# Kernel tuning notes

Measured on AMD Instinct MI355X. Metric: run time of the kernel, lower is better.

The kernel has to match this reference:

```python
import jax, jax.numpy as jnp
import numpy as np
from jax import lax


def _gru_layer(x, w_ih, w_hh, b_ih, b_hh):
    """PyTorch-style GRU layer (gate order r, z, n). x: [B,T,I] -> ([B,T,H], [B,H])."""
    B, T, _ = x.shape
    H = w_hh.shape[1]
    # Precompute all input-side gate projections in one big GEMM: [B,T,3H]
    xg = jnp.einsum('bti,gi->btg', x, w_ih) + b_ih

    def step(h, xg_t):
        hg = h @ w_hh.T + b_hh                      # [B,3H]
        xr, xz, xn = jnp.split(xg_t, 3, axis=-1)
        hr, hz, hn = jnp.split(hg, 3, axis=-1)
        r = jax.nn.sigmoid(xr + hr)
        z = jax.nn.sigmoid(xz + hz)
        n = jnp.tanh(xn + r * hn)
        h_new = (1.0 - z) * n + z * h
        return h_new, h_new

    h0 = jnp.zeros((B, H), dtype=x.dtype)
    h_last, hs = lax.scan(step, h0, jnp.swapaxes(xg, 0, 1))  # scan over time
    return jnp.swapaxes(hs, 0, 1), h_last


def setup_inputs() -> dict:
    key = jax.random.key(0)
    ks = jax.random.split(key, 13)
    B, T, I, H = 64, 512, 2048, 128

    def u(k, shape, fan_in):
        bound = 1.0 / np.sqrt(fan_in)
        return jax.random.uniform(k, shape, jnp.float32, -bound, bound)

    return {
        'x': jax.random.normal(ks[0], (B, T, I), jnp.float32),
        'w_ih0': u(ks[1], (3 * H, I), H),
        'w_hh0': u(ks[2], (3 * H, H), H),
        'b_ih0': u(ks[3], (3 * H,), H),
        'b_hh0': u(ks[4], (3 * H,), H),
        'w_ih1': u(ks[5], (3 * H, H), H),
        'w_hh1': u(ks[6], (3 * H, H), H),
        'b_ih1': u(ks[7], (3 * H,), H),
        'b_hh1': u(ks[8], (3 * H,), H),
        'w_fc1': u(ks[9], (64, H), H),
        'b_fc1': u(ks[10], (64,), H),
        'w_fc2': u(ks[11], (1, 64), 64),
        'b_fc2': u(ks[12], (1,), 64),
    }


def reference(x, w_ih0, w_hh0, b_ih0, b_hh0, w_ih1, w_hh1, b_ih1, b_hh1,
              w_fc1, b_fc1, w_fc2, b_fc2):
    # 2-layer GRU (inter-layer dropout is identity in eval mode)
    h1_seq, _ = _gru_layer(x, w_ih0, w_hh0, b_ih0, b_hh0)
    _, h_last = _gru_layer(h1_seq, w_ih1, w_hh1, b_ih1, b_hh1)
    # MLP head: fc1 -> ReLU -> (dropout=identity in eval) -> fc2
    y = jax.nn.relu(h_last @ w_fc1.T + b_fc1)
    return y @ w_fc2.T + b_fc2  # [B, 1]
```

## Files before the change

### kernel.cpp

```cpp
#include <hip/hip_runtime.h>
#include <cstdint>
#include <cstddef>

typedef float f32x4 __attribute__((ext_vector_type(4)));
typedef float f32x2 __attribute__((ext_vector_type(2)));
typedef short s16x8 __attribute__((ext_vector_type(8)));
typedef unsigned short u16;

static __device__ __forceinline__ u16 f2bf(float f) {
    uint32_t x = __float_as_uint(f);
    x += 0x7fffu + ((x >> 16) & 1u);
    return (u16)(x >> 16);
}
static __device__ __forceinline__ float bf2f(u16 h) {
    return __uint_as_float(((uint32_t)h) << 16);
}

static __device__ __forceinline__ void bar_lds() {
    asm volatile("s_waitcnt lgkmcnt(0)" ::: "memory");
    __builtin_amdgcn_s_barrier();
    asm volatile("" ::: "memory");
}

__global__ void k_zero(int* __restrict__ p, int n) {
    int i = blockIdx.x * 256 + threadIdx.x;
    if (i < n) p[i] = 0;
}

__global__ void k_split(const float* __restrict__ src, u16* __restrict__ hi,
                        u16* __restrict__ lo, int n) {
    int i = blockIdx.x * 256 + threadIdx.x;
    if (i < n) {
        float f = src[i];
        u16 h = f2bf(f);
        hi[i] = h;
        lo[i] = f2bf(f - bf2f(h));
    }
}

__global__ __launch_bounds__(256, 2)
void k_gemm(const float* __restrict__ A, const u16* __restrict__ Wh,
            const u16* __restrict__ Wl, const float* __restrict__ bias,
            float* __restrict__ C, int K) {
    __shared__ __align__(16) u16 sm[32768];

    const int tid  = threadIdx.x;
    const int lane = tid & 63;
    const int wave = tid >> 6;
    const int wm = wave >> 1, wn = wave & 1;

    int g = blockIdx.x;
    int xcd = g & 7, ix = g >> 3;
    int q3 = ix / 3;
    int mb = xcd + 8 * q3;
    int nb = ix - 3 * q3;
    const long m0 = (long)mb * 128;
    const int  n0 = nb * 128;

    f32x4 acc[4][4];
    const f32x4 vzero = {0.f, 0.f, 0.f, 0.f};
#pragma unroll
    for (int i = 0; i < 4; ++i)
#pragma unroll
        for (int j = 0; j < 4; ++j) acc[i][j] = vzero;

    const int ar = tid >> 1;
    const int ac = (tid & 1) * 16;
    const float* aptr = A + (m0 + ar) * (long)K + ac;
    const int br = tid >> 2;
    const int bc = (tid & 3) * 8;
    const u16* bhp = Wh + (long)(n0 + br) * K + bc;
    const u16* blp = Wl + (long)(n0 + br) * K + bc;

    const int ksteps = K >> 5;
    f32x4 a0, a1, a2, a3;

    {
        a0 = *(const f32x4*)(aptr + 0);
        a1 = *(const f32x4*)(aptr + 4);
        a2 = *(const f32x4*)(aptr + 8);
        a3 = *(const f32x4*)(aptr + 12);
#pragma unroll
        for (int c = 0; c < 2; ++c) {
            const u16* sh = bhp + (long)(c * 64) * K;
            const u16* sl = blp + (long)(c * 64) * K;
            u16* dh = &sm[8192  + c * 2048 + wave * 512];
            u16* dl = &sm[12288 + c * 2048 + wave * 512];
            __builtin_amdgcn_global_load_lds((const __attribute__((address_space(1))) void*)sh,
                                             (__attribute__((address_space(3))) void*)dh, 16, 0, 0);
            __builtin_amdgcn_global_load_lds((const __attribute__((address_space(1))) void*)sl,
                                             (__attribute__((address_space(3))) void*)dl, 16, 0, 0);
        }
        float fr[16] = {a0.x,a0.y,a0.z,a0.w, a1.x,a1.y,a1.z,a1.w,
                        a2.x,a2.y,a2.z,a2.w, a3.x,a3.y,a3.z,a3.w};
        s16x8 h0, h1, l0, l1;
#pragma unroll
        for (int i = 0; i < 8; ++i) {
            u16 hh = f2bf(fr[i]);     h0[i] = (short)hh; l0[i] = (short)f2bf(fr[i] - bf2f(hh));
            u16 hh2 = f2bf(fr[8+i]);  h1[i] = (short)hh2; l1[i] = (short)f2bf(fr[8+i] - bf2f(hh2));
        }
        u16* dh = &sm[ar * 32 + ac];
        u16* dl = &sm[4096 + ar * 32 + ac];
        *(s16x8*)dh = h0; *(s16x8*)(dh + 8) = h1;
        *(s16x8*)dl = l0; *(s16x8*)(dl + 8) = l1;
    }
    __syncthreads();

    for (int ks = 0; ks < ksteps; ++ks) {
        const int cur = ks & 1, nxt = cur ^ 1;
        const bool more = (ks + 1 < ksteps);
        if (more) {
            const int k0 = (ks + 1) << 5;
            a0 = *(const f32x4*)(aptr + k0 + 0);
            a1 = *(const f32x4*)(aptr + k0 + 4);
            a2 = *(const f32x4*)(aptr + k0 + 8);
            a3 = *(const f32x4*)(aptr + k0 + 12);
#pragma unroll
            for (int c = 0; c < 2; ++c) {
                const u16* sh = bhp + (long)(c * 64) * K + k0;
                const u16* sl = blp + (long)(c * 64) * K + k0;
                u16* dh = &sm[nxt * 16384 + 8192  + c * 2048 + wave * 512];
                u16* dl = &sm[nxt * 16384 + 12288 + c * 2048 + wave * 512];
                __builtin_amdgcn_global_load_lds((const __attribute__((address_space(1))) void*)sh,
                                                 (__attribute__((address_space(3))) void*)dh, 16, 0, 0);
                __builtin_amdgcn_global_load_lds((const __attribute__((address_space(1))) void*)sl,
                                                 (__attribute__((address_space(3))) void*)dl, 16, 0, 0);
            }
        }
        {
            const u16* base = &sm[cur * 16384];
            const int koff = (lane >> 4) * 8;
            const int rsel = lane & 15;
            s16x8 ah[4], al[4];
#pragma unroll
            for (int f = 0; f < 4; ++f) {
                int row = wm * 64 + f * 16 + rsel;
                ah[f] = *(const s16x8*)&base[row * 32 + koff];
                al[f] = *(const s16x8*)&base[4096 + row * 32 + koff];
            }
#pragma unroll
            for (int j = 0; j < 4; ++j) {
                int row = wn * 64 + j * 16 + rsel;
                s16x8 bh = *(const s16x8*)&base[8192  + row * 32 + koff];
                s16x8 bl = *(const s16x8*)&base[12288 + row * 32 + koff];
#pragma unroll
                for (int f = 0; f < 4; ++f) {
                    acc[f][j] = __builtin_amdgcn_mfma_f32_16x16x32_bf16(ah[f], bh, acc[f][j], 0, 0, 0);
                    acc[f][j] = __builtin_amdgcn_mfma_f32_16x16x32_bf16(ah[f], bl, acc[f][j], 0, 0, 0);
                    acc[f][j] = __builtin_amdgcn_mfma_f32_16x16x32_bf16(al[f], bh, acc[f][j], 0, 0, 0);
                }
            }
        }
        if (more) {
            float fr[16] = {a0.x,a0.y,a0.z,a0.w, a1.x,a1.y,a1.z,a1.w,
                            a2.x,a2.y,a2.z,a2.w, a3.x,a3.y,a3.z,a3.w};
            s16x8 h0, h1, l0, l1;
#pragma unroll
            for (int i = 0; i < 8; ++i) {
                u16 hh = f2bf(fr[i]);     h0[i] = (short)hh; l0[i] = (short)f2bf(fr[i] - bf2f(hh));
                u16 hh2 = f2bf(fr[8+i]);  h1[i] = (short)hh2; l1[i] = (short)f2bf(fr[8+i] - bf2f(hh2));
            }
            u16* dh = &sm[nxt * 16384 + ar * 32 + ac];
            u16* dl = &sm[nxt * 16384 + 4096 + ar * 32 + ac];
            *(s16x8*)dh = h0; *(s16x8*)(dh + 8) = h1;
            *(s16x8*)dl = l0; *(s16x8*)(dl + 8) = l1;
        }
        __syncthreads();
    }

    const int r0 = (lane >> 4) << 2;
    const int cn = lane & 15;
#pragma unroll
    for (int f = 0; f < 4; ++f) {
        const long mrow = m0 + wm * 64 + f * 16 + r0;
#pragma unroll
        for (int j = 0; j < 4; ++j) {
            const int n = n0 + wn * 64 + j * 16 + cn;
            const float bv = bias[n];
            float* o = C + mrow * 384 + n;
#pragma unroll
            for (int jj = 0; jj < 4; ++jj) o[(long)jj * 384] = acc[f][j][jj] + bv;
        }
    }
}


struct SmemRecur { float hsh[128]; float hp[8][384]; };
struct SmemGemm  { u16 ah[16 * 128]; u16 al[16 * 128]; };
union Smem {
    SmemRecur r;
    SmemGemm  g;
    char force_one_block_per_cu[98304];
};

#define R_ISSUE(BUF, G) do {                                                  \
    const int _G = (G);                                                       \
    if (_G < 128 && tid < 128) {                                              \
        if (!isL0 && (_G & 3) == 0) {                                         \
            if ((tid & 63) == 0) {                                            \
                while (atomicAdd(&waitflag[b * 32 + (_G >> 2)], 0) == 0)      \
                    __builtin_amdgcn_s_sleep(8);                              \
            }                                                                 \
            __threadfence();                                                  \
        }                                                                     \
        const float* _p = xgb + (size_t)(4 * _G) * 384 + tid;                 \
        BUF[0] = _p[0];    BUF[1] = _p[128];   BUF[2]  = _p[256];             \
        BUF[3] = _p[384];  BUF[4] = _p[512];   BUF[5]  = _p[640];             \
        BUF[6] = _p[768];  BUF[7] = _p[896];   BUF[8]  = _p[1024];            \
        BUF[9] = _p[1152]; BUF[10] = _p[1280]; BUF[11] = _p[1408];            \
    } } while (0)

#define R_STEP(T, BUF, J) do {                                                \
    const int _t = (T);                                                       \
    const f32x2 _h2 = *(const f32x2*)(sm.hsh + 2 * lane);                     \
    float _ha[16];                                                            \
    _Pragma("unroll")                                                         \
    for (int _i = 0; _i < 8; ++_i) {                                          \
        _ha[2 * _i] = __uint_as_float(                                        \
            __builtin_amdgcn_readlane(__float_as_uint(_h2[0]), rlx[_i]));     \
        _ha[2 * _i + 1] = __uint_as_float(                                    \
            __builtin_amdgcn_readlane(__float_as_uint(_h2[1]), rlx[_i]));     \
    }                                                                         \
    float _s0=0.f,_s1=0.f,_s2=0.f,_s3=0.f,_s4=0.f,_s5=0.f;                    \
    _Pragma("unroll")                                                         \
    for (int _i = 0; _i < 16; ++_i) {                                         \
        const float _hv = _ha[_i];                                            \
        _s0 = fmaf(_hv, wr[0][_i], _s0); _s1 = fmaf(_hv, wr[1][_i], _s1);     \
        _s2 = fmaf(_hv, wr[2][_i], _s2); _s3 = fmaf(_hv, wr[3][_i], _s3);     \
        _s4 = fmaf(_hv, wr[4][_i], _s4); _s5 = fmaf(_hv, wr[5][_i], _s5);     \
    }                                                                         \
    *(f32x2*)&sm.hp[w][g6 + 0] = (f32x2){_s0, _s1};                           \
    *(f32x2*)&sm.hp[w][g6 + 2] = (f32x2){_s2, _s3};                           \
    *(f32x2*)&sm.hp[w][g6 + 4] = (f32x2){_s4, _s5};                           \
    const bool _pub = isL0 && _t > 0 && (_t & 15) == 0;                       \
    if (_pub && tid < 128) asm volatile("s_waitcnt vmcnt(12)" ::: "memory");  \
    bar_lds();                                                                \
    if (_pub && tid == 0) {                                                   \
        __threadfence();                                                      \
        atomicExch(&setflag[b * 32 + ((_t >> 4) - 1)], 1);                    \
    }                                                                         \
    if (tid < 128) {                                                          \
        const int _c = tid;                                                   \
        float _hr = bhr, _hz = bhz, _hn = bhn;                                \
        _Pragma("unroll")                                                     \
        for (int _q = 0; _q < 8; ++_q) {                                      \
            _hr += sm.hp[_q][_c];                                             \
            _hz += sm.hp[_q][128 + _c];                                       \
            _hn += sm.hp[_q][256 + _c];                                       \
        }                                                                     \
        const float _xr = BUF[(J) * 3 + 0];                                   \
        const float _xz = BUF[(J) * 3 + 1];                                   \
        const float _xn = BUF[(J) * 3 + 2];                                   \
        const float _r = 1.f / (1.f + __expf(-(_xr + _hr)));                  \
        const float _z = 1.f / (1.f + __expf(-(_xz + _hz)));                  \
        float _a = _xn + _r * _hn;                                            \
        _a = fminf(fmaxf(_a, -15.f), 15.f);                                   \
        const float _e = __expf(2.f * _a);                                    \
        const float _n = (_e - 1.f) / (_e + 1.f);                             \
        hreg = (1.f - _z) * _n + _z * hreg;                                   \
        sm.hsh[_c] = hreg;                                                    \
        if (isL0) hseq[((size_t)(b * 512 + _t)) * 128 + _c] = hreg;           \
    }                                                                         \
    bar_lds();                                                                \
} while (0)

__device__ void recur_role(
    bool isL0, int b, const float* __restrict__ xg,
    const float* __restrict__ whh, const float* __restrict__ bhh,
    float* __restrict__ hseq, int* __restrict__ setflag, int* __restrict__ waitflag,
    const float* __restrict__ wfc1, const float* __restrict__ bfc1,
    const float* __restrict__ wfc2, const float* __restrict__ bfc2,
    float* __restrict__ out, SmemRecur& sm)
{
    const int tid  = threadIdx.x;
    const int w    = tid >> 6;
    const int lane = tid & 63;
    const int g6   = 6 * lane;

    int rlx[8];
#pragma unroll
    for (int k = 0; k < 8; ++k)
        rlx[k] = __builtin_amdgcn_readfirstlane(8 * w + k);

    float wr[6][16];
#pragma unroll
    for (int j = 0; j < 6; ++j) {
        const float* p = whh + (size_t)(g6 + j) * 128 + 16 * w;
#pragma unroll
        for (int i4 = 0; i4 < 4; ++i4) {
            f32x4 v = *(const f32x4*)(p + 4 * i4);
            wr[j][4*i4+0] = v[0]; wr[j][4*i4+1] = v[1];
            wr[j][4*i4+2] = v[2]; wr[j][4*i4+3] = v[3];
        }
    }
    float bhr = 0.f, bhz = 0.f, bhn = 0.f, hreg = 0.f;
    if (tid < 128) {
        bhr = bhh[tid]; bhz = bhh[128 + tid]; bhn = bhh[256 + tid];
        sm.hsh[tid] = 0.f;
    }
    const float* xgb = xg + (size_t)b * 512 * 384;

    float pA[12], pB[12];
    R_ISSUE(pA, 0);
    R_ISSUE(pB, 1);
    __syncthreads();

    for (int gp = 0; gp < 64; ++gp) {
        const int t0 = gp * 8;
        R_STEP(t0 + 0, pA, 0); R_STEP(t0 + 1, pA, 1);
        R_STEP(t0 + 2, pA, 2); R_STEP(t0 + 3, pA, 3);
        R_ISSUE(pA, 2 * gp + 2);
        R_STEP(t0 + 4, pB, 0); R_STEP(t0 + 5, pB, 1);
        R_STEP(t0 + 6, pB, 2); R_STEP(t0 + 7, pB, 3);
        R_ISSUE(pB, 2 * gp + 3);
    }

    if (isL0) {
        if (tid < 128) asm volatile("s_waitcnt vmcnt(0)" ::: "memory");
        __syncthreads();
        if (tid == 0) { __threadfence(); atomicExch(&setflag[b * 32 + 31], 1); }
    }

    if (!isL0 && tid < 64) {
        const float* wv = wfc1 + tid * 128;
        float acc = bfc1[tid];
#pragma unroll 8
        for (int c = 0; c < 128; ++c) acc = fmaf(sm.hsh[c], wv[c], acc);
        float p = fmaxf(acc, 0.f) * wfc2[tid];
#pragma unroll
        for (int off = 32; off > 0; off >>= 1) p += __shfl_down(p, off);
        if (tid == 0) out[b] = p + bfc2[0];
    }
}

__device__ void worker_role(
    int wk, const float* __restrict__ h1, float* __restrict__ xg,
    const float* __restrict__ wih1, const float* __restrict__ bih1,
    int* __restrict__ h1flag, int* __restrict__ xgflag, SmemGemm& sm)
{
    const int tid = threadIdx.x, lane = tid & 63, w = tid >> 6;
    const int rsel = lane & 15, koff = (lane >> 4) * 8;

    s16x8 bh[3][4], bl[3][4];
    float bias[3];
#pragma unroll
    for (int nfi = 0; nfi < 3; ++nfi) {
        const int n = (3 * w + nfi) * 16 + rsel;
        bias[nfi] = bih1[n];
#pragma unroll
        for (int ks = 0; ks < 4; ++ks) {
            const float* p = wih1 + n * 128 + ks * 32 + koff;
            f32x4 v0 = *(const f32x4*)p, v1 = *(const f32x4*)(p + 4);
            float fv[8] = {v0[0],v0[1],v0[2],v0[3], v1[0],v1[1],v1[2],v1[3]};
            s16x8 hh, ll;
#pragma unroll
            for (int i = 0; i < 8; ++i) {
                u16 h = f2bf(fv[i]); hh[i] = (short)h; ll[i] = (short)f2bf(fv[i] - bf2f(h));
            }
            bh[nfi][ks] = hh; bl[nfi][ks] = ll;
        }
    }

    for (int jt = wk; jt < 2048; jt += 128) {
        const int c = jt >> 6, b = jt & 63;
        if (tid == 0) {
            while (atomicAdd(&h1flag[b * 32 + c], 0) == 0) __builtin_amdgcn_s_sleep(8);
            __threadfence();
        }
        __syncthreads();
        if (tid < 256) {
            const int r = tid >> 4, c0 = (tid & 15) * 8;
            const float* p = h1 + ((size_t)(b * 512 + c * 16 + r)) * 128 + c0;
            f32x4 v0 = *(const f32x4*)p, v1 = *(const f32x4*)(p + 4);
            float fv[8] = {v0[0],v0[1],v0[2],v0[3], v1[0],v1[1],v1[2],v1[3]};
            s16x8 hh, ll;
#pragma unroll
            for (int i = 0; i < 8; ++i) {
                u16 h = f2bf(fv[i]); hh[i] = (short)h; ll[i] = (short)f2bf(fv[i] - bf2f(h));
            }
            const int sc = c0 ^ ((r & 7) << 3);
            *(s16x8*)&sm.ah[r * 128 + sc] = hh;
            *(s16x8*)&sm.al[r * 128 + sc] = ll;
        }
        __syncthreads();

        f32x4 acc[3];
        const f32x4 vz = {0.f, 0.f, 0.f, 0.f};
        acc[0] = vz; acc[1] = vz; acc[2] = vz;
#pragma unroll
        for (int ks = 0; ks < 4; ++ks) {
            const int si = rsel * 128 + ((ks * 32 + koff) ^ ((rsel & 7) << 3));
            s16x8 a_h = *(const s16x8*)&sm.ah[si];
            s16x8 a_l = *(const s16x8*)&sm.al[si];
#pragma unroll
            for (int nfi = 0; nfi < 3; ++nfi) {
                acc[nfi] = __builtin_amdgcn_mfma_f32_16x16x32_bf16(a_h, bh[nfi][ks], acc[nfi], 0, 0, 0);
                acc[nfi] = __builtin_amdgcn_mfma_f32_16x16x32_bf16(a_h, bl[nfi][ks], acc[nfi], 0, 0, 0);
                acc[nfi] = __builtin_amdgcn_mfma_f32_16x16x32_bf16(a_l, bh[nfi][ks], acc[nfi], 0, 0, 0);
            }
        }
#pragma unroll
        for (int nfi = 0; nfi < 3; ++nfi) {
            const int n = (3 * w + nfi) * 16 + rsel;
#pragma unroll
            for (int jj = 0; jj < 4; ++jj) {
                const int m = (lane >> 4) * 4 + jj;
                xg[((size_t)(b * 512 + c * 16 + m)) * 384 + n] = acc[nfi][jj] + bias[nfi];
            }
        }
        __syncthreads();
        if (tid == 0) {
            __threadfence();
            atomicExch(&xgflag[b * 32 + c], 1);
        }
    }
}

__global__ __launch_bounds__(512, 2)
void k_fused(float* __restrict__ xg, float* __restrict__ h1,
             const float* __restrict__ whh0, const float* __restrict__ bhh0,
             const float* __restrict__ wih1, const float* __restrict__ bih1,
             const float* __restrict__ whh1, const float* __restrict__ bhh1,
             const float* __restrict__ wfc1, const float* __restrict__ bfc1,
             const float* __restrict__ wfc2, const float* __restrict__ bfc2,
             float* __restrict__ out, int* __restrict__ h1flag, int* __restrict__ xgflag)
{
    __shared__ __align__(16) Smem sm;
    const int bid = blockIdx.x;
    if (bid < 64) {
        recur_role(true, bid, xg, whh0, bhh0, h1, h1flag, nullptr,
                   nullptr, nullptr, nullptr, nullptr, nullptr, sm.r);
    } else if (bid < 128) {
        recur_role(false, bid - 64, xg, whh1, bhh1, nullptr, nullptr, xgflag,
                   wfc1, bfc1, wfc2, bfc2, out, sm.r);
    } else {
        worker_role(bid - 128, h1, xg, wih1, bih1, h1flag, xgflag, sm.g);
    }
}

extern "C" void kernel_launch(void* const* d_in, const int* in_sizes, int n_in,
                              void* d_out, int out_size, void* d_ws, size_t ws_size,
                              hipStream_t stream) {
    const float* x     = (const float*)d_in[0];
    const float* w_ih0 = (const float*)d_in[1];
    const float* w_hh0 = (const float*)d_in[2];
    const float* b_ih0 = (const float*)d_in[3];
    const float* b_hh0 = (const float*)d_in[4];
    const float* w_ih1 = (const float*)d_in[5];
    const float* w_hh1 = (const float*)d_in[6];
    const float* b_ih1 = (const float*)d_in[7];
    const float* b_hh1 = (const float*)d_in[8];
    const float* w_fc1 = (const float*)d_in[9];
    const float* b_fc1 = (const float*)d_in[10];
    const float* w_fc2 = (const float*)d_in[11];
    const float* b_fc2 = (const float*)d_in[12];
    float* out = (float*)d_out;
    (void)in_sizes; (void)n_in; (void)out_size; (void)ws_size;

    char* ws = (char*)d_ws;
    float* xg     = (float*)(ws + 0);
    float* h1     = (float*)(ws + 50331648);
    u16*   w0h    = (u16*)(ws + 67108864);
    u16*   w0l    = (u16*)(ws + 68681728);
    int*   h1flag = (int*)(ws + 70254592);
    int*   xgflag = h1flag + 2048;

    k_zero<<<16, 256, 0, stream>>>(h1flag, 4096);
    k_split<<<3072, 256, 0, stream>>>(w_ih0, w0h, w0l, 384 * 2048);
    k_gemm<<<768, 256, 0, stream>>>(x, w0h, w0l, b_ih0, xg, 2048);
    k_fused<<<256, 512, 0, stream>>>(xg, h1, w_hh0, b_hh0, w_ih1, b_ih1,
                                     w_hh1, b_hh1, w_fc1, b_fc1, w_fc2, b_fc2,
                                     out, h1flag, xgflag);
}
```

Measured before the change: 689.2 us.

## Process two batch rows per recurrence block and give freed CUs to workers

Each recurrence block now advances two batch rows at once, so the 8 warps reuse their register-held W_hh slices for both rows. The h state is read by vector LDS loads instead of readlane broadcasts. Recurrence blocks drop from 128 to 64 and the worker stride grows to 192, so the freed CUs go to the layer-1 input-projection workers. Each step does twice the FMA work per block on the serial critical path, which may lengthen per-step latency.

```diff
diff --git a/kernel.cpp b/kernel.cpp
--- a/kernel.cpp
+++ b/kernel.cpp
@@ -185,7 +185,7 @@
 }
 
 
-struct SmemRecur { float hsh[128]; float hp[8][384]; };
+struct SmemRecur { float hsh[2][128]; float hp[2][8][384]; };
 struct SmemGemm  { u16 ah[16 * 128]; u16 al[16 * 128]; };
 union Smem {
     SmemRecur r;
@@ -195,15 +195,15 @@
 
 #define R_ISSUE(BUF, G) do {                                                  \
     const int _G = (G);                                                       \
-    if (_G < 128 && tid < 128) {                                              \
+    if (_G < 128 && tid < 256) {                                              \
         if (!isL0 && (_G & 3) == 0) {                                         \
             if ((tid & 63) == 0) {                                            \
-                while (atomicAdd(&waitflag[b * 32 + (_G >> 2)], 0) == 0)      \
+                while (atomicAdd(&waitflag[b2 * 32 + (_G >> 2)], 0) == 0)     \
                     __builtin_amdgcn_s_sleep(8);                              \
             }                                                                 \
             __threadfence();                                                  \
         }                                                                     \
-        const float* _p = xgb + (size_t)(4 * _G) * 384 + tid;                 \
+        const float* _p = xgb2 + (size_t)(4 * _G) * 384 + (tid & 127);        \
         BUF[0] = _p[0];    BUF[1] = _p[128];   BUF[2]  = _p[256];             \
         BUF[3] = _p[384];  BUF[4] = _p[512];   BUF[5]  = _p[640];             \
         BUF[6] = _p[768];  BUF[7] = _p[896];   BUF[8]  = _p[1024];            \
@@ -212,41 +212,44 @@
 
 #define R_STEP(T, BUF, J) do {                                                \
     const int _t = (T);                                                       \
-    const f32x2 _h2 = *(const f32x2*)(sm.hsh + 2 * lane);                     \
-    float _ha[16];                                                            \
     _Pragma("unroll")                                                         \
-    for (int _i = 0; _i < 8; ++_i) {                                          \
-        _ha[2 * _i] = __uint_as_float(                                        \
-            __builtin_amdgcn_readlane(__float_as_uint(_h2[0]), rlx[_i]));     \
-        _ha[2 * _i + 1] = __uint_as_float(                                    \
-            __builtin_amdgcn_readlane(__float_as_uint(_h2[1]), rlx[_i]));     \
+    for (int _bb = 0; _bb < 2; ++_bb) {                                       \
+        f32x4 _h0 = *(const f32x4*)(sm.hsh[_bb] + 16 * w + 0);                \
+        f32x4 _h1 = *(const f32x4*)(sm.hsh[_bb] + 16 * w + 4);                \
+        f32x4 _h2 = *(const f32x4*)(sm.hsh[_bb] + 16 * w + 8);                \
+        f32x4 _h3 = *(const f32x4*)(sm.hsh[_bb] + 16 * w + 12);               \
+        float _ha[16];                                                        \
+        _ha[0]=_h0[0];  _ha[1]=_h0[1];  _ha[2]=_h0[2];  _ha[3]=_h0[3];        \
+        _ha[4]=_h1[0];  _ha[5]=_h1[1];  _ha[6]=_h1[2];  _ha[7]=_h1[3];        \
+        _ha[8]=_h2[0];  _ha[9]=_h2[1];  _ha[10]=_h2[2]; _ha[11]=_h2[3];       \
+        _ha[12]=_h3[0]; _ha[13]=_h3[1]; _ha[14]=_h3[2]; _ha[15]=_h3[3];       \
+        float _s0=0.f,_s1=0.f,_s2=0.f,_s3=0.f,_s4=0.f,_s5=0.f;                \
+        _Pragma("unroll")                                                     \
+        for (int _i = 0; _i < 16; ++_i) {                                     \
+            const float _hv = _ha[_i];                                        \
+            _s0 = fmaf(_hv, wr[0][_i], _s0); _s1 = fmaf(_hv, wr[1][_i], _s1); \
+            _s2 = fmaf(_hv, wr[2][_i], _s2); _s3 = fmaf(_hv, wr[3][_i], _s3); \
+            _s4 = fmaf(_hv, wr[4][_i], _s4); _s5 = fmaf(_hv, wr[5][_i], _s5); \
+        }                                                                     \
+        *(f32x2*)&sm.hp[_bb][w][g6 + 0] = (f32x2){_s0, _s1};                  \
+        *(f32x2*)&sm.hp[_bb][w][g6 + 2] = (f32x2){_s2, _s3};                  \
+        *(f32x2*)&sm.hp[_bb][w][g6 + 4] = (f32x2){_s4, _s5};                  \
     }                                                                         \
-    float _s0=0.f,_s1=0.f,_s2=0.f,_s3=0.f,_s4=0.f,_s5=0.f;                    \
-    _Pragma("unroll")                                                         \
-    for (int _i = 0; _i < 16; ++_i) {                                         \
-        const float _hv = _ha[_i];                                            \
-        _s0 = fmaf(_hv, wr[0][_i], _s0); _s1 = fmaf(_hv, wr[1][_i], _s1);     \
-        _s2 = fmaf(_hv, wr[2][_i], _s2); _s3 = fmaf(_hv, wr[3][_i], _s3);     \
-        _s4 = fmaf(_hv, wr[4][_i], _s4); _s5 = fmaf(_hv, wr[5][_i], _s5);     \
+    const bool _pub = isL0 && _t > 0 && (_t & 15) == 0;                       \
+    if (_pub && tid < 256) asm volatile("s_waitcnt vmcnt(12)" ::: "memory");  \
+    bar_lds();                                                                \
+    if (_pub && (tid == 0 || tid == 128)) {                                   \
+        __threadfence();                                                      \
+        atomicExch(&setflag[b2 * 32 + ((_t >> 4) - 1)], 1);                   \
     }                                                                         \
-    *(f32x2*)&sm.hp[w][g6 + 0] = (f32x2){_s0, _s1};                           \
-    *(f32x2*)&sm.hp[w][g6 + 2] = (f32x2){_s2, _s3};                           \
-    *(f32x2*)&sm.hp[w][g6 + 4] = (f32x2){_s4, _s5};                           \
-    const bool _pub = isL0 && _t > 0 && (_t & 15) == 0;                       \
-    if (_pub && tid < 128) asm volatile("s_waitcnt vmcnt(12)" ::: "memory");  \
-    bar_lds();                                                                \
-    if (_pub && tid == 0) {                                                   \
-        __threadfence();                                                      \
-        atomicExch(&setflag[b * 32 + ((_t >> 4) - 1)], 1);                    \
-    }                                                                         \
-    if (tid < 128) {                                                          \
-        const int _c = tid;                                                   \
+    if (tid < 256) {                                                          \
+        const int _c = tid & 127;                                             \
         float _hr = bhr, _hz = bhz, _hn = bhn;                                \
         _Pragma("unroll")                                                     \
         for (int _q = 0; _q < 8; ++_q) {                                      \
-            _hr += sm.hp[_q][_c];                                             \
-            _hz += sm.hp[_q][128 + _c];                                       \
-            _hn += sm.hp[_q][256 + _c];                                       \
+            _hr += sm.hp[half][_q][_c];                                       \
+            _hz += sm.hp[half][_q][128 + _c];                                 \
+            _hn += sm.hp[half][_q][256 + _c];                                 \
         }                                                                     \
         const float _xr = BUF[(J) * 3 + 0];                                   \
         const float _xz = BUF[(J) * 3 + 1];                                   \
@@ -258,8 +261,8 @@
         const float _e = __expf(2.f * _a);                                    \
         const float _n = (_e - 1.f) / (_e + 1.f);                             \
         hreg = (1.f - _z) * _n + _z * hreg;                                   \
-        sm.hsh[_c] = hreg;                                                    \
-        if (isL0) hseq[((size_t)(b * 512 + _t)) * 128 + _c] = hreg;           \
+        sm.hsh[half][_c] = hreg;                                              \
+        if (isL0) hseq[((size_t)(b2 * 512 + _t)) * 128 + _c] = hreg;          \
     }                                                                         \
     bar_lds();                                                                \
 } while (0)
@@ -276,11 +279,8 @@
     const int w    = tid >> 6;
     const int lane = tid & 63;
     const int g6   = 6 * lane;
-
-    int rlx[8];
-#pragma unroll
-    for (int k = 0; k < 8; ++k)
-        rlx[k] = __builtin_amdgcn_readfirstlane(8 * w + k);
+    const int half = (tid >> 7) & 1;
+    const int b2   = 2 * b + half;
 
     float wr[6][16];
 #pragma unroll
@@ -294,11 +294,12 @@
         }
     }
     float bhr = 0.f, bhz = 0.f, bhn = 0.f, hreg = 0.f;
-    if (tid < 128) {
-        bhr = bhh[tid]; bhz = bhh[128 + tid]; bhn = bhh[256 + tid];
-        sm.hsh[tid] = 0.f;
-    }
-    const float* xgb = xg + (size_t)b * 512 * 384;
+    if (tid < 256) {
+        const int c = tid & 127;
+        bhr = bhh[c]; bhz = bhh[128 + c]; bhn = bhh[256 + c];
+        sm.hsh[half][c] = 0.f;
+    }
+    const float* xgb2 = xg + (size_t)b2 * 512 * 384;
 
     float pA[12], pB[12];
     R_ISSUE(pA, 0);
@@ -316,20 +317,28 @@
     }
 
     if (isL0) {
-        if (tid < 128) asm volatile("s_waitcnt vmcnt(0)" ::: "memory");
+        if (tid < 256) asm volatile("s_waitcnt vmcnt(0)" ::: "memory");
         __syncthreads();
-        if (tid == 0) { __threadfence(); atomicExch(&setflag[b * 32 + 31], 1); }
-    }
-
-    if (!isL0 && tid < 64) {
-        const float* wv = wfc1 + tid * 128;
-        float acc = bfc1[tid];
+        if (tid == 0 || tid == 128) {
+            __threadfence();
+            atomicExch(&setflag[b2 * 32 + 31], 1);
+        }
+    }
+
+    if (!isL0) {
+        const bool headw = (tid < 64) || (tid >= 128 && tid < 192);
+        if (headw) {
+            const int l_ = tid & 63;
+            const float* hv = sm.hsh[half];
+            const float* wv = wfc1 + l_ * 128;
+            float acc = bfc1[l_];
 #pragma unroll 8
-        for (int c = 0; c < 128; ++c) acc = fmaf(sm.hsh[c], wv[c], acc);
-        float p = fmaxf(acc, 0.f) * wfc2[tid];
-#pragma unroll
-        for (int off = 32; off > 0; off >>= 1) p += __shfl_down(p, off);
-        if (tid == 0) out[b] = p + bfc2[0];
+            for (int c = 0; c < 128; ++c) acc = fmaf(hv[c], wv[c], acc);
+            float p = fmaxf(acc, 0.f) * wfc2[l_];
+#pragma unroll
+            for (int off = 32; off > 0; off >>= 1) p += __shfl_down(p, off);
+            if (l_ == 0) out[b2] = p + bfc2[0];
+        }
     }
 }
 
@@ -361,7 +370,7 @@
         }
     }
 
-    for (int jt = wk; jt < 2048; jt += 128) {
+    for (int jt = wk; jt < 2048; jt += 192) {
         const int c = jt >> 6, b = jt & 63;
         if (tid == 0) {
             while (atomicAdd(&h1flag[b * 32 + c], 0) == 0) __builtin_amdgcn_s_sleep(8);
@@ -427,14 +436,14 @@
 {
     __shared__ __align__(16) Smem sm;
     const int bid = blockIdx.x;
-    if (bid < 64) {
+    if (bid < 32) {
         recur_role(true, bid, xg, whh0, bhh0, h1, h1flag, nullptr,
                    nullptr, nullptr, nullptr, nullptr, nullptr, sm.r);
-    } else if (bid < 128) {
-        recur_role(false, bid - 64, xg, whh1, bhh1, nullptr, nullptr, xgflag,
+    } else if (bid < 64) {
+        recur_role(false, bid - 32, xg, whh1, bhh1, nullptr, nullptr, xgflag,
                    wfc1, bfc1, wfc2, bfc2, out, sm.r);
     } else {
-        worker_role(bid - 128, h1, xg, wih1, bih1, h1flag, xgflag, sm.g);
+        worker_role(bid - 64, h1, xg, wih1, bih1, h1flag, xgflag, sm.g);
     }
 }
 
```

Measured after the change: 849.7 us. +23.3%, slower.
